# Kernel tuning notes

Measured on AMD Instinct MI355X. Metric: run time of the kernel, lower is better.

The kernel has to match this reference:

```python
import jax, jax.numpy as jnp
import numpy as np

B, C_IN, T = 256, 1024, 128   # batch, encoder channels, spectrogram frames (2**15 samples / 256 hop)
CTX, N_EVENTS = 64, 16        # context_dim, n_events (module constants)


def setup_inputs() -> dict:
    key = jax.random.key(0)
    k0, k1, k2 = jax.random.split(key, 3)
    return {
        "encoded": jax.random.normal(k0, (B, C_IN, T), dtype=jnp.float32),
        "w_vec": jax.random.normal(k1, (CTX, C_IN), dtype=jnp.float32) * 0.02,
        "b_vec": jnp.zeros((CTX,), dtype=jnp.float32),
        "w_switch": jax.random.normal(k2, (1, C_IN), dtype=jnp.float32) * 0.02,
        "b_switch": jnp.zeros((1,), dtype=jnp.float32),
    }


def reference(encoded, w_vec, b_vec, w_switch, b_switch):
    # 1x1 Conv1d == per-timestep matmul
    event_vecs = jnp.einsum('bct,dc->btd', encoded, w_vec) + b_vec          # [B,T,CTX]
    switch = jnp.einsum('bct,c->bt', encoded, w_switch[0]) + b_switch[0]    # [B,T]
    attn = jax.nn.relu(switch)                                              # [B,T]

    # sparsify: keep top-k attention values and their indices
    vals, idx = jax.lax.top_k(attn, N_EVENTS)                               # [B,K]

    # sparsify_vectors: gather event vectors at top-k time indices
    vecs = jnp.take_along_axis(event_vecs, idx[:, :, None], axis=1)         # [B,K,CTX]

    # scheduling[b, j, idx[b,j]] = attn[b, idx[b,j]] (vectorized scatter,
    # replaces the original nested python-loop scalar scatter)
    b_idx = jnp.arange(B)[:, None]
    j_idx = jnp.arange(N_EVENTS)[None, :]
    scheduling = jnp.zeros((B, N_EVENTS, T), dtype=attn.dtype)
    scheduling = scheduling.at[b_idx, j_idx, idx].set(vals)                 # [B,K,T]

    return vecs, scheduling
```

## Files before the change

### kernel.cpp

```cpp
#include <hip/hip_runtime.h>
#include <hip/hip_bf16.h>

#define C_IN 1024
#define T_SZ 128
#define CTX 64
#define NEV 16
#define BK 64
#define NTILE 16
#define NTHR 512
#define BROW 72
#define PLROW 132

#define BF_OFF 0
#define WB_OFF 36864
#define WS_OFF 55296
#define SP_OFF 59392
#define AT_OFF 63488
#define TV_OFF 64000
#define TI_OFF 64064
#define ARENA_SZ 64128

typedef short bf16x8 __attribute__((ext_vector_type(8)));
typedef float f32x4 __attribute__((ext_vector_type(4)));

__device__ __forceinline__ unsigned short f2bf(float f) {
  __hip_bfloat16 h = __float2bfloat16(f);
  return *(unsigned short*)&h;
}

#define BARRIER() do { \
  asm volatile("s_waitcnt lgkmcnt(0)" ::: "memory"); \
  __builtin_amdgcn_s_barrier(); \
} while (0)

#define ISSUE(kt, ev, wv) do { \
  const float* _s = encB + (kt) * (BK * T_SZ) + cb0 * T_SZ + t0; \
  _Pragma("unroll") for (int _j = 0; _j < 8; ++_j) \
    ev[_j] = *(const float2*)(_s + _j * T_SZ); \
  const float* _w = wvec + wd * C_IN + (kt) * BK + wc; \
  wv[0] = *(const float4*)_w; \
  wv[1] = *(const float4*)(_w + 4); \
} while (0)

#define CONVERT(kt, ev, wv, buf) do { \
  const float* _wt = wswl + (kt) * BK + cb0; \
  union { bf16x8 v; unsigned short u[8]; } _p0, _p1, _pw; \
  _Pragma("unroll") for (int _j = 0; _j < 8; ++_j) { \
    sw0 = fmaf(ev[_j].x, _wt[_j], sw0); \
    sw1 = fmaf(ev[_j].y, _wt[_j], sw1); \
    _p0.u[_j] = f2bf(ev[_j].x); \
    _p1.u[_j] = f2bf(ev[_j].y); \
  } \
  *(bf16x8*)&Bf[((buf) * T_SZ + t0) * BROW + cb0] = _p0.v; \
  *(bf16x8*)&Bf[((buf) * T_SZ + t0 + 1) * BROW + cb0] = _p1.v; \
  _pw.u[0] = f2bf(wv[0].x); _pw.u[1] = f2bf(wv[0].y); \
  _pw.u[2] = f2bf(wv[0].z); _pw.u[3] = f2bf(wv[0].w); \
  _pw.u[4] = f2bf(wv[1].x); _pw.u[5] = f2bf(wv[1].y); \
  _pw.u[6] = f2bf(wv[1].z); _pw.u[7] = f2bf(wv[1].w); \
  *(bf16x8*)&Wb[((buf) * CTX + wd) * BROW + wc] = _pw.v; \
} while (0)

#define MFMA_TILE(buf) do { \
  _Pragma("unroll") for (int _ks = 0; _ks < 2; ++_ks) { \
    bf16x8 _bv = *(const bf16x8*)&Bf[((buf) * T_SZ + n0 + tl) * BROW + _ks * 32 + g * 8]; \
    bf16x8 _a0 = *(const bf16x8*)&Wb[((buf) * CTX +  0 + tl) * BROW + _ks * 32 + g * 8]; \
    bf16x8 _a1 = *(const bf16x8*)&Wb[((buf) * CTX + 16 + tl) * BROW + _ks * 32 + g * 8]; \
    bf16x8 _a2 = *(const bf16x8*)&Wb[((buf) * CTX + 32 + tl) * BROW + _ks * 32 + g * 8]; \
    bf16x8 _a3 = *(const bf16x8*)&Wb[((buf) * CTX + 48 + tl) * BROW + _ks * 32 + g * 8]; \
    acc0 = __builtin_amdgcn_mfma_f32_16x16x32_bf16(_a0, _bv, acc0, 0, 0, 0); \
    acc1 = __builtin_amdgcn_mfma_f32_16x16x32_bf16(_a1, _bv, acc1, 0, 0, 0); \
    acc2 = __builtin_amdgcn_mfma_f32_16x16x32_bf16(_a2, _bv, acc2, 0, 0, 0); \
    acc3 = __builtin_amdgcn_mfma_f32_16x16x32_bf16(_a3, _bv, acc3, 0, 0, 0); \
  } } while (0)

#define STEP(T, SI, SC) do { \
  if ((T) + 3 < NTILE) ISSUE((T) + 3, ev##SI, wv##SI); \
  MFMA_TILE((T) & 1); \
  if ((T) + 1 < NTILE) CONVERT((T) + 1, ev##SC, wv##SC, ((T) + 1) & 1); \
  BARRIER(); \
} while (0)

__global__ __launch_bounds__(NTHR, 1) void fused_sparsify(
    const float* __restrict__ enc,
    const float* __restrict__ wvec,
    const float* __restrict__ bvec,
    const float* __restrict__ wsw,
    const float* __restrict__ bsw,
    float* __restrict__ out)
{
  const int b    = blockIdx.x;
  const int tid  = threadIdx.x;
  const int lane = tid & 63;
  const int wid  = tid >> 6;
  const int g    = lane >> 4;
  const int tl   = lane & 15;
  const int n0   = wid * 16;

  const int cb0 = wid * 8;
  const int t0  = 2 * lane;
  const int wd  = tid >> 3;
  const int wc  = (tid & 7) * 8;

  __shared__ __align__(16) char arena[ARENA_SZ];
  unsigned short* Bf = (unsigned short*)(arena + BF_OFF);
  unsigned short* Wb = (unsigned short*)(arena + WB_OFF);
  float* wswl = (float*)(arena + WS_OFF);
  float* swp  = (float*)(arena + SP_OFF);
  float* attn = (float*)(arena + AT_OFF);
  float* topv = (float*)(arena + TV_OFF);
  int*   topi = (int*)(arena + TI_OFF);

  const float* encB = enc + (size_t)b * (C_IN * T_SZ);

  f32x4 acc0 = {0.f, 0.f, 0.f, 0.f};
  f32x4 acc1 = acc0, acc2 = acc0, acc3 = acc0;
  float sw0 = 0.f, sw1 = 0.f;

  float2 evA[8], evB[8], evC[8];
  float4 wvA[2], wvB[2], wvC[2];

  ISSUE(0, evA, wvA);
  ISSUE(1, evB, wvB);
  ISSUE(2, evC, wvC);
  wswl[tid]       = wsw[tid];
  wswl[tid + 512] = wsw[tid + 512];
  BARRIER();
  CONVERT(0, evA, wvA, 0);
  BARRIER();

  STEP( 0, A, B); STEP( 1, B, C); STEP( 2, C, A);
  STEP( 3, A, B); STEP( 4, B, C); STEP( 5, C, A);
  STEP( 6, A, B); STEP( 7, B, C); STEP( 8, C, A);
  STEP( 9, A, B); STEP(10, B, C); STEP(11, C, A);
  STEP(12, A, B); STEP(13, B, C); STEP(14, C, A);
  MFMA_TILE(1);
  BARRIER();

  float* Pl = (float*)(arena + BF_OFF);
#pragma unroll
  for (int r = 0; r < 4; ++r) {
    Pl[( 0 + 4 * g + r) * PLROW + n0 + tl] = acc0[r];
    Pl[(16 + 4 * g + r) * PLROW + n0 + tl] = acc1[r];
    Pl[(32 + 4 * g + r) * PLROW + n0 + tl] = acc2[r];
    Pl[(48 + 4 * g + r) * PLROW + n0 + tl] = acc3[r];
  }
  swp[wid * T_SZ + t0]     = sw0;
  swp[wid * T_SZ + t0 + 1] = sw1;
  __syncthreads();

  if (tid < T_SZ) {
    float s = 0.f;
#pragma unroll
    for (int k = 0; k < 8; ++k) s += swp[k * T_SZ + tid];
    attn[tid] = fmaxf(s + bsw[0], 0.f);
  }
  __syncthreads();

  if (tid < 64) {
    float v0 = attn[tid], v1 = attn[tid + 64];
#pragma unroll 1
    for (int r = 0; r < NEV; ++r) {
      float bv; int bi;
      if (v0 >= v1) { bv = v0; bi = tid; } else { bv = v1; bi = tid + 64; }
#pragma unroll
      for (int off = 32; off > 0; off >>= 1) {
        float ov = __shfl_xor(bv, off, 64);
        int   oi = __shfl_xor(bi, off, 64);
        if (ov > bv || (ov == bv && oi < bi)) { bv = ov; bi = oi; }
      }
      if (bi == tid) v0 = -__builtin_inff();
      if (bi == tid + 64) v1 = -__builtin_inff();
      if (tid == r) { topv[r] = bv; topi[r] = bi; }
    }
  }
  __syncthreads();

  {
    float* os = out + (256 * NEV * CTX) + b * (NEV * T_SZ);
    int j  = tid >> 5;
    int tt = (tid * 4) & 127;
    float tv = topv[j];
    int   ti = topi[j];
    float4 v;
    v.x = (tt + 0 == ti) ? tv : 0.f;
    v.y = (tt + 1 == ti) ? tv : 0.f;
    v.z = (tt + 2 == ti) ? tv : 0.f;
    v.w = (tt + 3 == ti) ? tv : 0.f;
    *(float4*)&os[tid * 4] = v;
  }
  {
    float* ov = out + b * (NEV * CTX);
#pragma unroll
    for (int s = 0; s < 2; ++s) {
      int o = s * NTHR + tid;
      int j = o >> 6, d = o & 63;
      ov[o] = Pl[d * PLROW + topi[j]] + bvec[d];
    }
  }
}

extern "C" void kernel_launch(void* const* d_in, const int* in_sizes, int n_in,
                              void* d_out, int out_size, void* d_ws, size_t ws_size,
                              hipStream_t stream) {
  const float* enc  = (const float*)d_in[0];
  const float* wvec = (const float*)d_in[1];
  const float* bvec = (const float*)d_in[2];
  const float* wsw  = (const float*)d_in[3];
  const float* bsw  = (const float*)d_in[4];
  float* o = (float*)d_out;
  (void)in_sizes; (void)n_in; (void)out_size; (void)d_ws; (void)ws_size;
  fused_sparsify<<<256, NTHR, 0, stream>>>(enc, wvec, bvec, wsw, bsw, o);
}
```

Baseline: 35.72 us.

## Split waves into two ping-pong teams alternating load/convert and MFMA per tile

Doubles the block to 1024 threads and splits the waves into two teams. On each K-tile one team issues global loads and runs MFMAs while the other converts the next tile into LDS, so the teams alternate roles. Each team accumulates half the K tiles, and the partial products are summed in LDS before the top-k stage. The aim is more waves in flight to hide global load latency and to overlap conversion with matrix work. The cost is a shallower prefetch depth, an extra LDS reduction, and more register pressure from the higher thread count.

Measured after the change: 36.50 us. +2.2%, slower.

```diff
diff --git a/kernel.cpp b/kernel.cpp
--- a/kernel.cpp
+++ b/kernel.cpp
@@ -7,7 +7,7 @@
 #define NEV 16
 #define BK 64
 #define NTILE 16
-#define NTHR 512
+#define NTHR 1024
 #define BROW 72
 #define PLROW 132
 
@@ -15,10 +15,10 @@
 #define WB_OFF 36864
 #define WS_OFF 55296
 #define SP_OFF 59392
-#define AT_OFF 63488
-#define TV_OFF 64000
-#define TI_OFF 64064
-#define ARENA_SZ 64128
+#define AT_OFF 67584
+#define TV_OFF 68096
+#define TI_OFF 68160
+#define ARENA_SZ 68224
 
 typedef short bf16x8 __attribute__((ext_vector_type(8)));
 typedef float f32x4 __attribute__((ext_vector_type(4)));
@@ -32,6 +32,7 @@
   asm volatile("s_waitcnt lgkmcnt(0)" ::: "memory"); \
   __builtin_amdgcn_s_barrier(); \
 } while (0)
+#define SCHED0() __builtin_amdgcn_sched_barrier(0)
 
 #define ISSUE(kt, ev, wv) do { \
   const float* _s = encB + (kt) * (BK * T_SZ) + cb0 * T_SZ + t0; \
@@ -74,13 +75,16 @@
   } } while (0)
 
 #define STEP(T, SI, SC) do { \
-  if ((T) + 3 < NTILE) ISSUE((T) + 3, ev##SI, wv##SI); \
-  MFMA_TILE((T) & 1); \
-  if ((T) + 1 < NTILE) CONVERT((T) + 1, ev##SC, wv##SC, ((T) + 1) & 1); \
+  if (team == ((T) & 1)) { \
+    if ((T) + 2 < NTILE) { ISSUE((T) + 2, ev##SI, wv##SI); SCHED0(); } \
+    MFMA_TILE((T) & 1); \
+  } else if ((T) + 1 < NTILE) { \
+    CONVERT((T) + 1, ev##SC, wv##SC, ((T) + 1) & 1); \
+  } \
   BARRIER(); \
 } while (0)
 
-__global__ __launch_bounds__(NTHR, 1) void fused_sparsify(
+__global__ __launch_bounds__(NTHR, 4) void fused_sparsify(
     const float* __restrict__ enc,
     const float* __restrict__ wvec,
     const float* __restrict__ bvec,
@@ -92,14 +96,17 @@
   const int tid  = threadIdx.x;
   const int lane = tid & 63;
   const int wid  = tid >> 6;
+  const int team = wid & 1;
+  const int vw   = wid >> 1;
   const int g    = lane >> 4;
   const int tl   = lane & 15;
-  const int n0   = wid * 16;
-
-  const int cb0 = wid * 8;
+  const int n0   = vw * 16;
+
+  const int cb0 = vw * 8;
   const int t0  = 2 * lane;
-  const int wd  = tid >> 3;
-  const int wc  = (tid & 7) * 8;
+  const int tt  = vw * 64 + lane;
+  const int wd  = tt >> 3;
+  const int wc  = (tt & 7) * 8;
 
   __shared__ __align__(16) char arena[ARENA_SZ];
   unsigned short* Bf = (unsigned short*)(arena + BF_OFF);
@@ -116,42 +123,48 @@
   f32x4 acc1 = acc0, acc2 = acc0, acc3 = acc0;
   float sw0 = 0.f, sw1 = 0.f;
 
-  float2 evA[8], evB[8], evC[8];
-  float4 wvA[2], wvB[2], wvC[2];
-
-  ISSUE(0, evA, wvA);
-  ISSUE(1, evB, wvB);
-  ISSUE(2, evC, wvC);
-  wswl[tid]       = wsw[tid];
-  wswl[tid + 512] = wsw[tid + 512];
+  float2 evX[8], evY[8];
+  float4 wvX[2], wvY[2];
+
+  ISSUE(team, evX, wvX);
+  SCHED0();
+  wswl[tid] = wsw[tid];
   BARRIER();
-  CONVERT(0, evA, wvA, 0);
+  if (team == 0) CONVERT(0, evX, wvX, 0);
   BARRIER();
 
-  STEP( 0, A, B); STEP( 1, B, C); STEP( 2, C, A);
-  STEP( 3, A, B); STEP( 4, B, C); STEP( 5, C, A);
-  STEP( 6, A, B); STEP( 7, B, C); STEP( 8, C, A);
-  STEP( 9, A, B); STEP(10, B, C); STEP(11, C, A);
-  STEP(12, A, B); STEP(13, B, C); STEP(14, C, A);
-  MFMA_TILE(1);
-  BARRIER();
+  STEP( 0, Y, X); STEP( 1, Y, Y); STEP( 2, X, Y); STEP( 3, X, X);
+  STEP( 4, Y, X); STEP( 5, Y, Y); STEP( 6, X, Y); STEP( 7, X, X);
+  STEP( 8, Y, X); STEP( 9, Y, Y); STEP(10, X, Y); STEP(11, X, X);
+  STEP(12, Y, X); STEP(13, Y, Y); STEP(14, X, Y); STEP(15, X, X);
 
   float* Pl = (float*)(arena + BF_OFF);
-#pragma unroll
-  for (int r = 0; r < 4; ++r) {
-    Pl[( 0 + 4 * g + r) * PLROW + n0 + tl] = acc0[r];
-    Pl[(16 + 4 * g + r) * PLROW + n0 + tl] = acc1[r];
-    Pl[(32 + 4 * g + r) * PLROW + n0 + tl] = acc2[r];
-    Pl[(48 + 4 * g + r) * PLROW + n0 + tl] = acc3[r];
+  if (team == 1) {
+#pragma unroll
+    for (int r = 0; r < 4; ++r) {
+      Pl[( 0 + 4 * g + r) * PLROW + n0 + tl] = acc0[r];
+      Pl[(16 + 4 * g + r) * PLROW + n0 + tl] = acc1[r];
+      Pl[(32 + 4 * g + r) * PLROW + n0 + tl] = acc2[r];
+      Pl[(48 + 4 * g + r) * PLROW + n0 + tl] = acc3[r];
+    }
   }
   swp[wid * T_SZ + t0]     = sw0;
   swp[wid * T_SZ + t0 + 1] = sw1;
   __syncthreads();
 
+  if (team == 0) {
+#pragma unroll
+    for (int r = 0; r < 4; ++r) {
+      Pl[( 0 + 4 * g + r) * PLROW + n0 + tl] += acc0[r];
+      Pl[(16 + 4 * g + r) * PLROW + n0 + tl] += acc1[r];
+      Pl[(32 + 4 * g + r) * PLROW + n0 + tl] += acc2[r];
+      Pl[(48 + 4 * g + r) * PLROW + n0 + tl] += acc3[r];
+    }
+  }
   if (tid < T_SZ) {
     float s = 0.f;
 #pragma unroll
-    for (int k = 0; k < 8; ++k) s += swp[k * T_SZ + tid];
+    for (int k = 0; k < 16; ++k) s += swp[k * T_SZ + tid];
     attn[tid] = fmaxf(s + bsw[0], 0.f);
   }
   __syncthreads();
@@ -177,25 +190,19 @@
 
   {
     float* os = out + (256 * NEV * CTX) + b * (NEV * T_SZ);
-    int j  = tid >> 5;
-    int tt = (tid * 4) & 127;
+    int j   = tid >> 6;
+    int tt2 = (tid * 2) & 127;
     float tv = topv[j];
     int   ti = topi[j];
-    float4 v;
-    v.x = (tt + 0 == ti) ? tv : 0.f;
-    v.y = (tt + 1 == ti) ? tv : 0.f;
-    v.z = (tt + 2 == ti) ? tv : 0.f;
-    v.w = (tt + 3 == ti) ? tv : 0.f;
-    *(float4*)&os[tid * 4] = v;
+    float2 v;
+    v.x = (tt2 + 0 == ti) ? tv : 0.f;
+    v.y = (tt2 + 1 == ti) ? tv : 0.f;
+    *(float2*)&os[tid * 2] = v;
   }
   {
     float* ov = out + b * (NEV * CTX);
-#pragma unroll
-    for (int s = 0; s < 2; ++s) {
-      int o = s * NTHR + tid;
-      int j = o >> 6, d = o & 63;
-      ov[o] = Pl[d * PLROW + topi[j]] + bvec[d];
-    }
+    int j = tid >> 6, d = tid & 63;
+    ov[tid] = Pl[d * PLROW + topi[j]] + bvec[d];
   }
 }
 
```
